# Kernel tuning notes

Hardware: AMD Instinct MI355X
Metric: run time of the kernel (lower is better)

The kernel has to match this reference:

```python
import jax, jax.numpy as jnp
from jax import lax
import numpy as np

MAXLEN, B, D = 2048, 64, 256
CONV_CH = 512

def setup_inputs() -> dict:
    key = jax.random.key(0)
    ks = jax.random.split(key, 10)
    inp = {
        "ctx_val": jax.random.normal(ks[0], (MAXLEN, B, D), jnp.float32),
        "ctx_key": jax.random.normal(ks[1], (MAXLEN, B, D), jnp.float32),
        "ctx_mask": jnp.ones((MAXLEN, B), jnp.float32),
        "attention_past": jax.random.uniform(ks[2], (B, 1, MAXLEN), jnp.float32),
        "ht_query": jax.random.normal(ks[3], (B, D), jnp.float32),
        # learned parameters (torch default inits approximated with scaled normals)
        "W_conv": jax.random.normal(ks[4], (CONV_CH, 1, 3), jnp.float32) * (1.0 / np.sqrt(3.0)),
        "W_query": jax.random.normal(ks[5], (D, D), jnp.float32) * (1.0 / np.sqrt(D)),
        "W_att_past": jax.random.normal(ks[6], (D, CONV_CH), jnp.float32) * (1.0 / np.sqrt(CONV_CH)),
        "b_att_past": jax.random.normal(ks[7], (D,), jnp.float32) * 0.01,
        "W_attn": jax.random.normal(ks[8], (1, D), jnp.float32) * (1.0 / np.sqrt(D)),
        "b_attn": jax.random.normal(ks[9], (1,), jnp.float32) * 0.01,
    }
    return inp

def reference(ctx_val, ctx_key, ctx_mask, attention_past, ht_query,
              W_conv, W_query, W_att_past, b_att_past, W_attn, b_attn):
    # fc_query: (b, D)
    hq = ht_query @ W_query.T
    # conv1d(1->512, k=3, pad=1, no bias): (b, 512, L)
    ap = lax.conv_general_dilated(attention_past, W_conv, window_strides=(1,),
                                  padding=[(1, 1)],
                                  dimension_numbers=("NCH", "OIH", "NCH"))
    # permute(2,0,1) -> (L, b, 512), then fc_att_past -> (L, b, D)
    ap = jnp.einsum("blc,dc->lbd", jnp.transpose(ap, (2, 0, 1)).transpose(1, 0, 2), W_att_past) + b_att_past
    # additive attention score: (L, b)
    s = jnp.tanh(ctx_key + hq[None, :, :] + ap)
    score = jnp.einsum("lbd,d->lb", s, W_attn[0]) + b_attn[0]
    # hard threshold mask, normalize over seq dim
    hard = (score >= 0).astype(jnp.float32) * ctx_mask
    hard = hard / (hard.sum(axis=0) + 1e-10)
    # masked weighted sum over seq dim: (b, D)
    ct = jnp.einsum("lbd,lb->bd", ctx_val, hard)
    return (ct, hard)
```

## Files before the change

### kernel.cpp

```cpp
#include <hip/hip_runtime.h>
#include <math.h>

#define L_MAX 2048
#define BATCH 64
#define DIM   256
#define CCH   512
#define ROWSTRIDE (BATCH * DIM)

#define HQ_OFF   0
#define WF_OFF   16384
#define SUMS_OFF 17152
#define HARD_OFF 19200
#define PART_OFF 150272
#define SUMS_STRIDE 32

__device__ __forceinline__ float fast_tanh(float x) {
    float ax = fabsf(x);
    float e  = __expf(2.0f * ax);
    float r  = 1.0f - 2.0f * __builtin_amdgcn_rcpf(e + 1.0f);
    return copysignf(r, x);
}

__global__ __launch_bounds__(256) void prep_kernel(
    const float* __restrict__ ht_query, const float* __restrict__ W_query,
    const float* __restrict__ W_conv,   const float* __restrict__ W_att_past,
    float* __restrict__ hq, float* __restrict__ wf, float* __restrict__ sums) {
    int t   = threadIdx.x;
    int blk = blockIdx.x;
    if (blk == 0 && t < BATCH) sums[t * SUMS_STRIDE] = 0.f;
    __shared__ float q[DIM];
    if (blk < BATCH) {
        q[t] = ht_query[blk * DIM + t];
        __syncthreads();
        const float4* wrow = (const float4*)(W_query + t * DIM);
        float acc = 0.f;
        #pragma unroll 8
        for (int k = 0; k < DIM / 4; k++) {
            float4 wv = wrow[k];
            acc += q[4*k] * wv.x + q[4*k+1] * wv.y + q[4*k+2] * wv.z + q[4*k+3] * wv.w;
        }
        hq[blk * DIM + t] = acc;
    } else {
        int j = blk - BATCH;
        const float4* wrow = (const float4*)(W_att_past + t * CCH);
        float acc = 0.f;
        #pragma unroll 8
        for (int c = 0; c < CCH / 4; c++) {
            float4 wv = wrow[c];
            acc += W_conv[(4*c  ) * 3 + j] * wv.x + W_conv[(4*c+1) * 3 + j] * wv.y
                 + W_conv[(4*c+2) * 3 + j] * wv.z + W_conv[(4*c+3) * 3 + j] * wv.w;
        }
        wf[j * DIM + t] = acc;
    }
}

__global__ __launch_bounds__(256) void fused_kernel(
    const float* __restrict__ ctx_key, const float* __restrict__ ctx_val,
    const float* __restrict__ ctx_mask, const float* __restrict__ att_past,
    const float* __restrict__ hq, const float* __restrict__ wf,
    const float* __restrict__ b_att_past, const float* __restrict__ W_attn,
    const float* __restrict__ b_attn,
    float* __restrict__ hard_raw, float* __restrict__ sums,
    float* __restrict__ part) {
    int b     = blockIdx.x & 63;
    int chunk = blockIdx.x >> 6;
    int w     = threadIdx.x >> 6;
    int lane  = threadIdx.x & 63;
    int d0    = lane << 2;
    int l0    = chunk * 64 + w * 16;

    float4 hq4 = *(const float4*)(hq + b * DIM + d0);
    float4 bp  = *(const float4*)(b_att_past + d0);
    hq4.x += bp.x; hq4.y += bp.y; hq4.z += bp.z; hq4.w += bp.w;
    float4 w0  = *(const float4*)(wf + d0);
    float4 w1  = *(const float4*)(wf + DIM + d0);
    float4 w2  = *(const float4*)(wf + 2 * DIM + d0);
    float4 wa  = *(const float4*)(W_attn + d0);
    float battn = b_attn[0];
    const float* apb = att_past + b * L_MAX;

    float ap[18];
    {
        float4 t0 = *(const float4*)(apb + l0);
        float4 t1 = *(const float4*)(apb + l0 + 4);
        float4 t2 = *(const float4*)(apb + l0 + 8);
        float4 t3 = *(const float4*)(apb + l0 + 12);
        ap[1]=t0.x; ap[2]=t0.y; ap[3]=t0.z; ap[4]=t0.w;
        ap[5]=t1.x; ap[6]=t1.y; ap[7]=t1.z; ap[8]=t1.w;
        ap[9]=t2.x; ap[10]=t2.y; ap[11]=t2.z; ap[12]=t2.w;
        ap[13]=t3.x; ap[14]=t3.y; ap[15]=t3.z; ap[16]=t3.w;
        ap[0]  = (l0 > 0)          ? apb[l0 - 1]  : 0.f;
        ap[17] = (l0 + 16 < L_MAX) ? apb[l0 + 16] : 0.f;
    }

    const float* key_base = ctx_key + (size_t)(l0 * BATCH + b) * DIM + d0;
    const float* val_base = ctx_val + (size_t)(l0 * BATCH + b) * DIM + d0;

    float4 k16[16];
    float m16[16];
    #pragma unroll
    for (int j = 0; j < 16; j++)
        k16[j] = *(const float4*)(key_base + (size_t)j * ROWSTRIDE);
    #pragma unroll
    for (int j = 0; j < 16; j++)
        m16[j] = ctx_mask[(l0 + j) * BATCH + b];

    float p[16];
    #pragma unroll
    for (int j = 0; j < 16; j++) {
        float am = ap[j], a0 = ap[j + 1], a1 = ap[j + 2];
        float x0 = k16[j].x + hq4.x + am * w0.x + a0 * w1.x + a1 * w2.x;
        float x1 = k16[j].y + hq4.y + am * w0.y + a0 * w1.y + a1 * w2.y;
        float x2 = k16[j].z + hq4.z + am * w0.z + a0 * w1.z + a1 * w2.z;
        float x3 = k16[j].w + hq4.w + am * w0.w + a0 * w1.w + a1 * w2.w;
        p[j] = fast_tanh(x0) * wa.x + fast_tanh(x1) * wa.y +
               fast_tanh(x2) * wa.z + fast_tanh(x3) * wa.w;
    }
    #pragma unroll
    for (int off = 32; off > 0; off >>= 1) {
        #pragma unroll
        for (int j = 0; j < 16; j++)
            p[j] += __shfl_xor(p[j], off, 64);
    }

    float h[16];
    float cnt = 0.f;
    #pragma unroll
    for (int j = 0; j < 16; j++) {
        h[j] = (p[j] + battn >= 0.f) ? m16[j] : 0.f;
        cnt += h[j];
    }
    if (lane == 0) {
        #pragma unroll
        for (int j = 0; j < 16; j++)
            hard_raw[(l0 + j) * BATCH + b] = h[j];
    }

    float4 acc = make_float4(0.f, 0.f, 0.f, 0.f);
    float4 v16[16];
    #pragma unroll
    for (int j = 0; j < 16; j++) {
        size_t off = (h[j] != 0.f) ? (size_t)j * ROWSTRIDE : 0;
        v16[j] = *(const float4*)(val_base + off);
    }
    #pragma unroll
    for (int j = 0; j < 16; j++) {
        acc.x += v16[j].x * h[j]; acc.y += v16[j].y * h[j];
        acc.z += v16[j].z * h[j]; acc.w += v16[j].w * h[j];
    }

    __shared__ float red[4 * DIM];
    *(float4*)(red + w * DIM + d0) = acc;
    __shared__ float c4[4];
    if (lane == 0) c4[w] = cnt;
    __syncthreads();
    int d = threadIdx.x;
    float s = red[d] + red[DIM + d] + red[2 * DIM + d] + red[3 * DIM + d];
    part[(size_t)(chunk * BATCH + b) * DIM + d] = s;
    if (threadIdx.x == 0)
        atomicAdd(&sums[b * SUMS_STRIDE], c4[0] + c4[1] + c4[2] + c4[3]);
}

__global__ __launch_bounds__(256) void tail_kernel(
    const float* __restrict__ part, const float* __restrict__ hard_raw,
    const float* __restrict__ sums,
    float* __restrict__ ct, float* __restrict__ out_hard) {
    if (blockIdx.x < BATCH) {
        int b = blockIdx.x;
        int d = threadIdx.x;
        float s = 0.f;
        #pragma unroll 8
        for (int c = 0; c < 32; c++)
            s += part[(size_t)(c * BATCH + b) * DIM + d];
        float invZ = 1.0f / (sums[b * SUMS_STRIDE] + 1e-10f);
        ct[b * DIM + d] = s * invZ;
    } else {
        int i = (blockIdx.x - BATCH) * 256 + threadIdx.x;
        float4 h = *(const float4*)(hard_raw + (size_t)i * 4);
        int b0 = (i * 4) & 63;
        float4 o;
        o.x = h.x / (sums[(b0 + 0) * SUMS_STRIDE] + 1e-10f);
        o.y = h.y / (sums[(b0 + 1) * SUMS_STRIDE] + 1e-10f);
        o.z = h.z / (sums[(b0 + 2) * SUMS_STRIDE] + 1e-10f);
        o.w = h.w / (sums[(b0 + 3) * SUMS_STRIDE] + 1e-10f);
        *(float4*)(out_hard + (size_t)i * 4) = o;
    }
}

extern "C" void kernel_launch(void* const* d_in, const int* in_sizes, int n_in,
                              void* d_out, int out_size, void* d_ws, size_t ws_size,
                              hipStream_t stream) {
    const float* ctx_val    = (const float*)d_in[0];
    const float* ctx_key    = (const float*)d_in[1];
    const float* ctx_mask   = (const float*)d_in[2];
    const float* att_past   = (const float*)d_in[3];
    const float* ht_query   = (const float*)d_in[4];
    const float* W_conv     = (const float*)d_in[5];
    const float* W_query    = (const float*)d_in[6];
    const float* W_att_past = (const float*)d_in[7];
    const float* b_att_past = (const float*)d_in[8];
    const float* W_attn     = (const float*)d_in[9];
    const float* b_attn     = (const float*)d_in[10];

    float* ws   = (float*)d_ws;
    float* hq   = ws + HQ_OFF;
    float* wf   = ws + WF_OFF;
    float* sums = ws + SUMS_OFF;
    float* hard = ws + HARD_OFF;
    float* part = ws + PART_OFF;

    float* out_ct   = (float*)d_out;
    float* out_hard = (float*)d_out + BATCH * DIM;

    prep_kernel<<<BATCH + 3, 256, 0, stream>>>(
        ht_query, W_query, W_conv, W_att_past, hq, wf, sums);

    fused_kernel<<<BATCH * 32, 256, 0, stream>>>(
        ctx_key, ctx_val, ctx_mask, att_past, hq, wf, b_att_past, W_attn, b_attn,
        hard, sums, part);

    tail_kernel<<<BATCH + 128, 256, 0, stream>>>(part, hard, sums, out_ct, out_hard);
}
```

Baseline: 323.3 us.

## Stream key/value rows through LDS with async global_load_lds double-stage pipeline

Replaces the register-held batch of 16 key and value float4 loads with direct global-to-LDS loads issued in groups of 4 rows. The next key group is prefetched while the current one is scored, and value rows are loaded only for rows that pass the mask. The aim is to cut VGPR pressure so occupancy rises, and to overlap memory with tanh compute. In exchange it adds a block-wide __syncthreads on every step and serialises score and accumulate into four phases, which may reduce memory-level parallelism. Reusing kbuf for the prefetch while other waves may still be reading it looks like a race, because the only barrier comes after the issue.

```diff
diff --git a/kernel.cpp b/kernel.cpp
--- a/kernel.cpp
+++ b/kernel.cpp
@@ -19,6 +19,13 @@
     float e  = __expf(2.0f * ax);
     float r  = 1.0f - 2.0f * __builtin_amdgcn_rcpf(e + 1.0f);
     return copysignf(r, x);
+}
+
+__device__ __forceinline__ void gload16(const float* g, float* l) {
+    __builtin_amdgcn_global_load_lds(
+        (const __attribute__((address_space(1))) void*)g,
+        (__attribute__((address_space(3))) void*)l,
+        16, 0, 0);
 }
 
 __global__ __launch_bounds__(256) void prep_kernel(
@@ -62,12 +69,17 @@
     const float* __restrict__ b_attn,
     float* __restrict__ hard_raw, float* __restrict__ sums,
     float* __restrict__ part) {
+    __shared__ float kbuf[16 * DIM];
+    __shared__ float vbuf[16 * DIM];
+    __shared__ float red[4 * DIM];
+    __shared__ float c4[4];
+
     int b     = blockIdx.x & 63;
     int chunk = blockIdx.x >> 6;
     int w     = threadIdx.x >> 6;
     int lane  = threadIdx.x & 63;
     int d0    = lane << 2;
-    int l0    = chunk * 64 + w * 16;
+    int l0w   = chunk * 64 + w * 16;
 
     float4 hq4 = *(const float4*)(hq + b * DIM + d0);
     float4 bp  = *(const float4*)(b_att_past + d0);
@@ -81,82 +93,97 @@
 
     float ap[18];
     {
-        float4 t0 = *(const float4*)(apb + l0);
-        float4 t1 = *(const float4*)(apb + l0 + 4);
-        float4 t2 = *(const float4*)(apb + l0 + 8);
-        float4 t3 = *(const float4*)(apb + l0 + 12);
+        float4 t0 = *(const float4*)(apb + l0w);
+        float4 t1 = *(const float4*)(apb + l0w + 4);
+        float4 t2 = *(const float4*)(apb + l0w + 8);
+        float4 t3 = *(const float4*)(apb + l0w + 12);
         ap[1]=t0.x; ap[2]=t0.y; ap[3]=t0.z; ap[4]=t0.w;
         ap[5]=t1.x; ap[6]=t1.y; ap[7]=t1.z; ap[8]=t1.w;
         ap[9]=t2.x; ap[10]=t2.y; ap[11]=t2.z; ap[12]=t2.w;
         ap[13]=t3.x; ap[14]=t3.y; ap[15]=t3.z; ap[16]=t3.w;
-        ap[0]  = (l0 > 0)          ? apb[l0 - 1]  : 0.f;
-        ap[17] = (l0 + 16 < L_MAX) ? apb[l0 + 16] : 0.f;
-    }
-
-    const float* key_base = ctx_key + (size_t)(l0 * BATCH + b) * DIM + d0;
-    const float* val_base = ctx_val + (size_t)(l0 * BATCH + b) * DIM + d0;
-
-    float4 k16[16];
+        ap[0]  = (l0w > 0)          ? apb[l0w - 1]  : 0.f;
+        ap[17] = (l0w + 16 < L_MAX) ? apb[l0w + 16] : 0.f;
+    }
+
     float m16[16];
     #pragma unroll
     for (int j = 0; j < 16; j++)
-        k16[j] = *(const float4*)(key_base + (size_t)j * ROWSTRIDE);
+        m16[j] = ctx_mask[(l0w + j) * BATCH + b];
+
     #pragma unroll
-    for (int j = 0; j < 16; j++)
-        m16[j] = ctx_mask[(l0 + j) * BATCH + b];
-
-    float p[16];
+    for (int j = 0; j < 4; j++)
+        gload16(ctx_key + (size_t)((l0w + j) * BATCH + b) * DIM + d0,
+                &kbuf[(w * 4 + j) * DIM]);
+    __syncthreads();
+
+    float h16[16];
+    float cnt = 0.f;
+    float4 acc = make_float4(0.f, 0.f, 0.f, 0.f);
+
     #pragma unroll
-    for (int j = 0; j < 16; j++) {
-        float am = ap[j], a0 = ap[j + 1], a1 = ap[j + 2];
-        float x0 = k16[j].x + hq4.x + am * w0.x + a0 * w1.x + a1 * w2.x;
-        float x1 = k16[j].y + hq4.y + am * w0.y + a0 * w1.y + a1 * w2.y;
-        float x2 = k16[j].z + hq4.z + am * w0.z + a0 * w1.z + a1 * w2.z;
-        float x3 = k16[j].w + hq4.w + am * w0.w + a0 * w1.w + a1 * w2.w;
-        p[j] = fast_tanh(x0) * wa.x + fast_tanh(x1) * wa.y +
-               fast_tanh(x2) * wa.z + fast_tanh(x3) * wa.w;
-    }
-    #pragma unroll
-    for (int off = 32; off > 0; off >>= 1) {
+    for (int s = 0; s < 4; s++) {
+        float p[4];
+        #pragma unroll
+        for (int j = 0; j < 4; j++) {
+            int r = 4 * s + j;
+            float4 k = *(const float4*)&kbuf[(w * 4 + j) * DIM + d0];
+            float am = ap[r], a0 = ap[r + 1], a1 = ap[r + 2];
+            float x0 = k.x + hq4.x + am * w0.x + a0 * w1.x + a1 * w2.x;
+            float x1 = k.y + hq4.y + am * w0.y + a0 * w1.y + a1 * w2.y;
+            float x2 = k.z + hq4.z + am * w0.z + a0 * w1.z + a1 * w2.z;
+            float x3 = k.w + hq4.w + am * w0.w + a0 * w1.w + a1 * w2.w;
+            p[j] = fast_tanh(x0) * wa.x + fast_tanh(x1) * wa.y +
+                   fast_tanh(x2) * wa.z + fast_tanh(x3) * wa.w;
+        }
+        #pragma unroll
+        for (int off = 32; off > 0; off >>= 1) {
+            #pragma unroll
+            for (int j = 0; j < 4; j++)
+                p[j] += __shfl_xor(p[j], off, 64);
+        }
+        #pragma unroll
+        for (int j = 0; j < 4; j++) {
+            h16[4 * s + j] = (p[j] + battn >= 0.f) ? m16[4 * s + j] : 0.f;
+            cnt += h16[4 * s + j];
+        }
+
+        #pragma unroll
+        for (int j = 0; j < 4; j++) {
+            if (h16[4 * s + j] != 0.f)
+                gload16(ctx_val + (size_t)((l0w + 4 * s + j) * BATCH + b) * DIM + d0,
+                        &vbuf[(w * 4 + j) * DIM]);
+        }
+        if (s < 3) {
+            #pragma unroll
+            for (int j = 0; j < 4; j++)
+                gload16(ctx_key + (size_t)((l0w + 4 * (s + 1) + j) * BATCH + b) * DIM + d0,
+                        &kbuf[(w * 4 + j) * DIM]);
+        }
+        __syncthreads();
+
+        #pragma unroll
+        for (int j = 0; j < 4; j++) {
+            float hv = h16[4 * s + j];
+            if (hv != 0.f) {
+                float4 v = *(const float4*)&vbuf[(w * 4 + j) * DIM + d0];
+                acc.x += v.x * hv; acc.y += v.y * hv;
+                acc.z += v.z * hv; acc.w += v.w * hv;
+            }
+        }
+    }
+
+    if (lane == 0) {
         #pragma unroll
         for (int j = 0; j < 16; j++)
-            p[j] += __shfl_xor(p[j], off, 64);
-    }
-
-    float h[16];
-    float cnt = 0.f;
-    #pragma unroll
-    for (int j = 0; j < 16; j++) {
-        h[j] = (p[j] + battn >= 0.f) ? m16[j] : 0.f;
-        cnt += h[j];
-    }
-    if (lane == 0) {
-        #pragma unroll
-        for (int j = 0; j < 16; j++)
-            hard_raw[(l0 + j) * BATCH + b] = h[j];
-    }
-
-    float4 acc = make_float4(0.f, 0.f, 0.f, 0.f);
-    float4 v16[16];
-    #pragma unroll
-    for (int j = 0; j < 16; j++) {
-        size_t off = (h[j] != 0.f) ? (size_t)j * ROWSTRIDE : 0;
-        v16[j] = *(const float4*)(val_base + off);
-    }
-    #pragma unroll
-    for (int j = 0; j < 16; j++) {
-        acc.x += v16[j].x * h[j]; acc.y += v16[j].y * h[j];
-        acc.z += v16[j].z * h[j]; acc.w += v16[j].w * h[j];
-    }
-
-    __shared__ float red[4 * DIM];
+            hard_raw[(l0w + j) * BATCH + b] = h16[j];
+    }
+
     *(float4*)(red + w * DIM + d0) = acc;
-    __shared__ float c4[4];
     if (lane == 0) c4[w] = cnt;
     __syncthreads();
     int d = threadIdx.x;
-    float s = red[d] + red[DIM + d] + red[2 * DIM + d] + red[3 * DIM + d];
-    part[(size_t)(chunk * BATCH + b) * DIM + d] = s;
+    float sred = red[d] + red[DIM + d] + red[2 * DIM + d] + red[3 * DIM + d];
+    part[(size_t)(chunk * BATCH + b) * DIM + d] = sred;
     if (threadIdx.x == 0)
         atomicAdd(&sums[b * SUMS_STRIDE], c4[0] + c4[1] + c4[2] + c4[3]);
 }
```

Measured after the change: 322.4 us. No clear change (-0.3%).
